# Performance work log

Measured on AMD Instinct MI355X. Metric: run time of the kernel, lower is better.

## Reference

```python
import jax, jax.numpy as jnp
import numpy as np
from functools import partial

N_NODES = 50000
N_EDGES = 800000
EMBED_DIM = 128
NUM_GROUPS = 3
T = 1.0


def setup_inputs() -> dict:
    key = jax.random.key(0)
    k1, k2, k3, k4 = jax.random.split(key, 4)
    node_feature = jax.random.normal(k1, (N_NODES, EMBED_DIM), dtype=jnp.float32)
    src = jax.random.randint(k2, (N_EDGES,), 0, N_NODES, dtype=jnp.int32)
    dst = jax.random.randint(k3, (N_EDGES,), 0, N_NODES, dtype=jnp.int32)
    W = jax.random.normal(k4, (EMBED_DIM, NUM_GROUPS), dtype=jnp.float32) / np.sqrt(EMBED_DIM)
    b = jnp.zeros((NUM_GROUPS,), dtype=jnp.float32)
    return {"node_feature": node_feature, "src": src, "dst": dst, "W": W, "b": b}


def reference(node_feature, src, dst, W, b):
    n = node_feature.shape[0]
    # linear + softmax group scores: [N, G]
    coeff = jax.nn.softmax((node_feature @ W + b) / T, axis=1)
    # weighted individual features: [N, G, D]
    wif = node_feature[:, None, :] * coeff[:, :, None]
    # message: gather src features per edge; reduce: mean over in-neighbors
    summed = jax.ops.segment_sum(wif[src], dst, num_segments=n)  # [N, G, D]
    deg = jax.ops.segment_sum(jnp.ones_like(dst, dtype=node_feature.dtype), dst, num_segments=n)
    group_feat = summed / jnp.maximum(deg, 1.0)[:, None, None]  # mean; zero-degree -> 0
    # weighted sum over groups with destination's own incidence coeff: [N, D]
    weighted_group_feat = jnp.einsum('ngd,ng->nd', group_feat, coeff)
    return weighted_group_feat
```

## Files before the change

### kernel.cpp

```cpp
#include <hip/hip_runtime.h>
#include <hip/hip_bf16.h>

#define D 128
#define G 3
#define BN 128
#define CH 8192
#define BIN_T 1024
#define CAP 4096
#define REG 8192

__global__ __launch_bounds__(256) void lg_coeff_kernel(
        const float* __restrict__ X, const float* __restrict__ W,
        const float* __restrict__ b, float4* __restrict__ coeff,
        __hip_bfloat16* __restrict__ Xh,
        int* __restrict__ cursor, int nbuck,
        int n) {
    if (cursor && blockIdx.x == 0) {
        for (int i = threadIdx.x; i < nbuck; i += 256) cursor[i] = 0;
    }
    int node = (int)((blockIdx.x * (size_t)blockDim.x + threadIdx.x) >> 6);
    int lane = threadIdx.x & 63;
    if (node >= n) return;
    float2 x = ((const float2*)(X + (size_t)node * D))[lane];
    if (Xh) {
        __hip_bfloat162 h2;
        h2.x = __float2bfloat16(x.x);
        h2.y = __float2bfloat16(x.y);
        ((__hip_bfloat162*)(Xh + (size_t)node * D))[lane] = h2;
    }
    int d0 = lane * 2;
    float s0 = x.x * W[d0 * G + 0] + x.y * W[(d0 + 1) * G + 0];
    float s1 = x.x * W[d0 * G + 1] + x.y * W[(d0 + 1) * G + 1];
    float s2 = x.x * W[d0 * G + 2] + x.y * W[(d0 + 1) * G + 2];
    #pragma unroll
    for (int off = 32; off; off >>= 1) {
        s0 += __shfl_xor(s0, off);
        s1 += __shfl_xor(s1, off);
        s2 += __shfl_xor(s2, off);
    }
    s0 += b[0]; s1 += b[1]; s2 += b[2];
    float m = fmaxf(s0, fmaxf(s1, s2));
    float e0 = __expf(s0 - m), e1 = __expf(s1 - m), e2 = __expf(s2 - m);
    float inv = 1.0f / (e0 + e1 + e2);
    if (lane == 0) coeff[node] = make_float4(e0 * inv, e1 * inv, e2 * inv, 0.0f);
}

__global__ __launch_bounds__(BIN_T) void lg_bin_kernel(
        const int* __restrict__ src, const int* __restrict__ dst,
        int* __restrict__ cursor, unsigned int* __restrict__ temp,
        int E, int nbuck) {
    __shared__ unsigned int stage[CH];
    __shared__ int hist[512], hbase[512], hcnt[512], gbs[512];
    int tid = threadIdx.x;
    int wv = tid >> 6, ln = tid & 63;
    int e0 = blockIdx.x * CH;
    int ecnt = min(CH, E - e0);
    for (int i = tid; i < 512; i += BIN_T) { hist[i] = 0; hcnt[i] = 0; }
    __syncthreads();
    int rs[CH / BIN_T], rd[CH / BIN_T];
    #pragma unroll
    for (int u = 0; u < CH / BIN_T; ++u) {
        int k = tid + u * BIN_T;
        if (k < ecnt) {
            rs[u] = src[e0 + k];
            rd[u] = dst[e0 + k];
            atomicAdd(&hist[rd[u] >> 7], 1);
        } else rd[u] = -1;
    }
    __syncthreads();
    if (wv == 0) {
        int c[8]; int tot = 0;
        #pragma unroll
        for (int t = 0; t < 8; ++t) { c[t] = hist[ln * 8 + t]; tot += c[t]; }
        int s = tot;
        #pragma unroll
        for (int o = 1; o < 64; o <<= 1) {
            int y = __shfl_up(s, o);
            if (ln >= o) s += y;
        }
        int run = s - tot;
        #pragma unroll
        for (int t = 0; t < 8; ++t) { hbase[ln * 8 + t] = run; run += c[t]; }
    }
    __syncthreads();
    #pragma unroll
    for (int u = 0; u < CH / BIN_T; ++u) {
        if (rd[u] >= 0) {
            int bk = rd[u] >> 7;
            int idx = hbase[bk] + atomicAdd(&hcnt[bk], 1);
            stage[idx] = ((unsigned int)rs[u] & 0xFFFFu) |
                         (((unsigned int)rd[u] & 127u) << 16);
        }
    }
    for (int i = tid; i < nbuck; i += BIN_T) {
        int c = hist[i];
        gbs[i] = c ? atomicAdd(&cursor[i], c) : 0;
    }
    __syncthreads();
    for (int bk = wv; bk < nbuck; bk += BIN_T / 64) {
        int c = hist[bk];
        if (!c) continue;
        int gb = gbs[bk], hb = hbase[bk];
        unsigned int* rg = temp + (size_t)bk * REG;
        int lim = min(c, REG - gb);
        for (int j = ln; j < lim; j += 64) rg[gb + j] = stage[hb + j];
    }
}

__global__ __launch_bounds__(1024) void lg_sortagg_kernel(
        const __hip_bfloat16* __restrict__ Xh,
        const float4* __restrict__ coeff,
        const unsigned int* __restrict__ temp,
        const int* __restrict__ cursor,
        float* __restrict__ out, int n) {
    __shared__ unsigned int stage[CAP];
    __shared__ float4 cdl[BN];
    __shared__ int nhist[BN], nbase[BN], ncur[BN];
    int tid = threadIdx.x;
    int wv = tid >> 6, ln = tid & 63;
    int nb0 = blockIdx.x * BN;
    int nv = min(BN, n - nb0);
    const unsigned int* rg = temp + (size_t)blockIdx.x * REG;
    int count = min(cursor[blockIdx.x], REG);
    if (tid < BN) { nhist[tid] = 0; ncur[tid] = 0; }
    if (tid < nv) cdl[tid] = coeff[nb0 + tid];
    __syncthreads();

    if (count <= CAP) {
        int k0 = tid, k1 = tid + 1024, k2 = tid + 2048, k3 = tid + 3072;
        unsigned int r0 = 0, r1 = 0, r2 = 0, r3 = 0;
        if (k0 < count) { r0 = rg[k0]; atomicAdd(&nhist[(r0 >> 16) & 127u], 1); }
        if (k1 < count) { r1 = rg[k1]; atomicAdd(&nhist[(r1 >> 16) & 127u], 1); }
        if (k2 < count) { r2 = rg[k2]; atomicAdd(&nhist[(r2 >> 16) & 127u], 1); }
        if (k3 < count) { r3 = rg[k3]; atomicAdd(&nhist[(r3 >> 16) & 127u], 1); }
        __syncthreads();
        if (wv == 0) {
            int a = nhist[2 * ln], b2 = nhist[2 * ln + 1];
            int tot = a + b2;
            int s = tot;
            #pragma unroll
            for (int o = 1; o < 64; o <<= 1) {
                int y = __shfl_up(s, o);
                if (ln >= o) s += y;
            }
            int excl = s - tot;
            nbase[2 * ln] = excl;
            nbase[2 * ln + 1] = excl + a;
        }
        __syncthreads();
        auto place = [&](unsigned int rec) {
            int s = (int)(rec & 0xFFFFu);
            int d = (int)((rec >> 16) & 127u);
            float4 cs = coeff[s];
            float4 cd = cdl[d];
            float w = cs.x * cd.x + cs.y * cd.y + cs.z * cd.z;
            unsigned int wb = __float_as_uint(w);
            wb += 0x7FFFu + ((wb >> 16) & 1u);
            int pos = nbase[d] + atomicAdd(&ncur[d], 1);
            stage[pos] = (rec & 0xFFFFu) | (wb & 0xFFFF0000u);
        };
        if (k0 < count) place(r0);
        if (k1 < count) place(r1);
        if (k2 < count) place(r2);
        if (k3 < count) place(r3);
        __syncthreads();
        for (int i = wv; i < nv; i += 16) {
            int ibeg = nbase[i];
            int icnt = nhist[i];
            float accx = 0.0f, accy = 0.0f;
            int j = 0;
            for (; j + 7 < icnt; j += 8) {
                unsigned int q0 = stage[ibeg + j + 0];
                unsigned int q1 = stage[ibeg + j + 1];
                unsigned int q2 = stage[ibeg + j + 2];
                unsigned int q3 = stage[ibeg + j + 3];
                unsigned int q4 = stage[ibeg + j + 4];
                unsigned int q5 = stage[ibeg + j + 5];
                unsigned int q6 = stage[ibeg + j + 6];
                unsigned int q7 = stage[ibeg + j + 7];
                __hip_bfloat162 h0 = ((const __hip_bfloat162*)(Xh + (size_t)(q0 & 0xFFFFu) * D))[ln];
                __hip_bfloat162 h1 = ((const __hip_bfloat162*)(Xh + (size_t)(q1 & 0xFFFFu) * D))[ln];
                __hip_bfloat162 h2 = ((const __hip_bfloat162*)(Xh + (size_t)(q2 & 0xFFFFu) * D))[ln];
                __hip_bfloat162 h3 = ((const __hip_bfloat162*)(Xh + (size_t)(q3 & 0xFFFFu) * D))[ln];
                __hip_bfloat162 h4 = ((const __hip_bfloat162*)(Xh + (size_t)(q4 & 0xFFFFu) * D))[ln];
                __hip_bfloat162 h5 = ((const __hip_bfloat162*)(Xh + (size_t)(q5 & 0xFFFFu) * D))[ln];
                __hip_bfloat162 h6 = ((const __hip_bfloat162*)(Xh + (size_t)(q6 & 0xFFFFu) * D))[ln];
                __hip_bfloat162 h7 = ((const __hip_bfloat162*)(Xh + (size_t)(q7 & 0xFFFFu) * D))[ln];
                float w0 = __uint_as_float(q0 & 0xFFFF0000u);
                float w1 = __uint_as_float(q1 & 0xFFFF0000u);
                float w2 = __uint_as_float(q2 & 0xFFFF0000u);
                float w3 = __uint_as_float(q3 & 0xFFFF0000u);
                float w4 = __uint_as_float(q4 & 0xFFFF0000u);
                float w5 = __uint_as_float(q5 & 0xFFFF0000u);
                float w6 = __uint_as_float(q6 & 0xFFFF0000u);
                float w7 = __uint_as_float(q7 & 0xFFFF0000u);
                accx = fmaf(w0, __bfloat162float(h0.x), accx);
                accy = fmaf(w0, __bfloat162float(h0.y), accy);
                accx = fmaf(w1, __bfloat162float(h1.x), accx);
                accy = fmaf(w1, __bfloat162float(h1.y), accy);
                accx = fmaf(w2, __bfloat162float(h2.x), accx);
                accy = fmaf(w2, __bfloat162float(h2.y), accy);
                accx = fmaf(w3, __bfloat162float(h3.x), accx);
                accy = fmaf(w3, __bfloat162float(h3.y), accy);
                accx = fmaf(w4, __bfloat162float(h4.x), accx);
                accy = fmaf(w4, __bfloat162float(h4.y), accy);
                accx = fmaf(w5, __bfloat162float(h5.x), accx);
                accy = fmaf(w5, __bfloat162float(h5.y), accy);
                accx = fmaf(w6, __bfloat162float(h6.x), accx);
                accy = fmaf(w6, __bfloat162float(h6.y), accy);
                accx = fmaf(w7, __bfloat162float(h7.x), accx);
                accy = fmaf(w7, __bfloat162float(h7.y), accy);
            }
            for (; j < icnt; ++j) {
                unsigned int q0 = stage[ibeg + j];
                int s0 = (int)(q0 & 0xFFFFu);
                float w0 = __uint_as_float(q0 & 0xFFFF0000u);
                __hip_bfloat162 h0 = ((const __hip_bfloat162*)(Xh + (size_t)s0 * D))[ln];
                accx = fmaf(w0, __bfloat162float(h0.x), accx);
                accy = fmaf(w0, __bfloat162float(h0.y), accy);
            }
            float invd = 1.0f / fmaxf((float)icnt, 1.0f);
            ((float2*)(out + (size_t)(nb0 + i) * D))[ln] =
                make_float2(accx * invd, accy * invd);
        }
    } else {
        for (int k = tid; k < count; k += 1024)
            atomicAdd(&nhist[(rg[k] >> 16) & 127u], 1);
        __syncthreads();
        for (int i = wv; i < nv; i += 16) {
            float4 cd = cdl[i];
            float accx = 0.0f, accy = 0.0f;
            for (int base = 0; base < count; base += 64) {
                int k = base + ln;
                unsigned int rec = (k < count) ? rg[k] : 0u;
                bool ok = (k < count) && ((int)((rec >> 16) & 127u) == i);
                unsigned long long mask = __ballot(ok);
                while (mask) {
                    int bpos = __ffsll((long long)mask) - 1;
                    mask &= mask - 1;
                    unsigned int rr = __shfl(rec, bpos);
                    int s0 = (int)(rr & 0xFFFFu);
                    float4 cs = coeff[s0];
                    float w = cs.x * cd.x + cs.y * cd.y + cs.z * cd.z;
                    __hip_bfloat162 h0 = ((const __hip_bfloat162*)(Xh + (size_t)s0 * D))[ln];
                    accx = fmaf(w, __bfloat162float(h0.x), accx);
                    accy = fmaf(w, __bfloat162float(h0.y), accy);
                }
            }
            float invd = 1.0f / fmaxf((float)nhist[i], 1.0f);
            ((float2*)(out + (size_t)(nb0 + i) * D))[ln] =
                make_float2(accx * invd, accy * invd);
        }
    }
}

__global__ void lg_deg_kernel(const int* __restrict__ dst, int* __restrict__ deg, int E) {
    int e = (int)(blockIdx.x * (size_t)blockDim.x + threadIdx.x);
    if (e < E) atomicAdd(&deg[dst[e]], 1);
}

__global__ void lg_scatter_kernel(const float* __restrict__ X,
                                  const float4* __restrict__ coeff,
                                  const int* __restrict__ src, const int* __restrict__ dst,
                                  float* __restrict__ out, int E) {
    int e = (int)((blockIdx.x * (size_t)blockDim.x + threadIdx.x) >> 6);
    int lane = threadIdx.x & 63;
    if (e >= E) return;
    int s = src[e], d = dst[e];
    float4 cs = coeff[s], cd = coeff[d];
    float se = cs.x * cd.x + cs.y * cd.y + cs.z * cd.z;
    float2 x = ((const float2*)(X + (size_t)s * D))[lane];
    atomicAdd(&out[(size_t)d * D + lane * 2 + 0], se * x.x);
    atomicAdd(&out[(size_t)d * D + lane * 2 + 1], se * x.y);
}

__global__ void lg_scale_kernel(float* __restrict__ out, const int* __restrict__ deg, int n) {
    int node = (int)((blockIdx.x * (size_t)blockDim.x + threadIdx.x) >> 6);
    int lane = threadIdx.x & 63;
    if (node >= n) return;
    float invd = 1.0f / fmaxf((float)deg[node], 1.0f);
    float2* p = (float2*)(out + (size_t)node * D);
    float2 v = p[lane];
    p[lane] = make_float2(v.x * invd, v.y * invd);
}

extern "C" void kernel_launch(void* const* d_in, const int* in_sizes, int n_in,
                              void* d_out, int out_size, void* d_ws, size_t ws_size,
                              hipStream_t stream) {
    const float* X   = (const float*)d_in[0];
    const int*   src = (const int*)d_in[1];
    const int*   dst = (const int*)d_in[2];
    const float* W   = (const float*)d_in[3];
    const float* b   = (const float*)d_in[4];
    float* out = (float*)d_out;
    int n = in_sizes[0] / D;
    int E = in_sizes[1];

    int nbuck  = (n + BN - 1) / BN;
    int nchunk = (E + CH - 1) / CH;

    char* ws = (char*)d_ws;
    size_t p = 0;
    auto alloc = [&](size_t bytes) -> void* {
        void* r = ws + p;
        p = (p + bytes + 255) & ~(size_t)255;
        return r;
    };
    float4* coeff  = (float4*)alloc((size_t)n * sizeof(float4));
    int*    cursor = (int*)alloc((size_t)nbuck * sizeof(int));
    unsigned int* temp = (unsigned int*)alloc((size_t)nbuck * REG * sizeof(unsigned int));
    __hip_bfloat16* Xh = (__hip_bfloat16*)alloc((size_t)n * D * sizeof(__hip_bfloat16));
    size_t p_full = p;
    int*    deg    = (int*)alloc((size_t)n * sizeof(int));

    int node_blocks = (n + 3) / 4;
    int edge_blocks = (E + 255) / 256;

    bool fast_ok = (n <= 65536) && (nbuck <= 512) && (p_full <= ws_size);
    if (fast_ok) {
        lg_coeff_kernel<<<node_blocks, 256, 0, stream>>>(X, W, b, coeff, Xh,
                                                         cursor, nbuck, n);
        lg_bin_kernel<<<nchunk, BIN_T, 0, stream>>>(src, dst, cursor, temp, E, nbuck);
        lg_sortagg_kernel<<<nbuck, 1024, 0, stream>>>(Xh, coeff, temp, cursor, out, n);
    } else {
        hipMemsetAsync(deg, 0, (size_t)n * sizeof(int), stream);
        hipMemsetAsync(out, 0, (size_t)n * D * sizeof(float), stream);
        lg_coeff_kernel<<<node_blocks, 256, 0, stream>>>(X, W, b, coeff, nullptr,
                                                         nullptr, 0, n);
        lg_deg_kernel<<<edge_blocks, 256, 0, stream>>>(dst, deg, E);
        lg_scatter_kernel<<<(E + 3) / 4, 256, 0, stream>>>(X, coeff, src, dst, out, E);
        lg_scale_kernel<<<node_blocks, 256, 0, stream>>>(out, deg, n);
    }
}
```

Before: 69.15 us.

## Split wave into half-waves gathering two edges with 8-byte bf16 loads

The aggregation loop now has each half-wave (32 lanes) gather a different source row with ushort4 loads, so each wave processes two edges per load instruction, then combines halves with a cross-lane shuffle before a float4 store. Bin records are loaded as uint4 per thread instead of strided scalar loads, and the binning chunk/thread constants are halved. The aim is fewer, wider memory instructions per edge, at the cost of a shuffle reduction and half the lanes idle on the store. The odd-count tail pads with a zero-weight record.

```diff
diff --git a/kernel.cpp b/kernel.cpp
--- a/kernel.cpp
+++ b/kernel.cpp
@@ -4,10 +4,14 @@
 #define D 128
 #define G 3
 #define BN 128
-#define CH 8192
-#define BIN_T 1024
+#define CH 4096
+#define BIN_T 512
 #define CAP 4096
 #define REG 8192
+
+__device__ __forceinline__ float b2f(unsigned short u) {
+    return __uint_as_float((unsigned int)u << 16);
+}
 
 __global__ __launch_bounds__(256) void lg_coeff_kernel(
         const float* __restrict__ X, const float* __restrict__ W,
@@ -127,12 +131,21 @@
     __syncthreads();
 
     if (count <= CAP) {
-        int k0 = tid, k1 = tid + 1024, k2 = tid + 2048, k3 = tid + 3072;
+        int base = tid * 4;
         unsigned int r0 = 0, r1 = 0, r2 = 0, r3 = 0;
-        if (k0 < count) { r0 = rg[k0]; atomicAdd(&nhist[(r0 >> 16) & 127u], 1); }
-        if (k1 < count) { r1 = rg[k1]; atomicAdd(&nhist[(r1 >> 16) & 127u], 1); }
-        if (k2 < count) { r2 = rg[k2]; atomicAdd(&nhist[(r2 >> 16) & 127u], 1); }
-        if (k3 < count) { r3 = rg[k3]; atomicAdd(&nhist[(r3 >> 16) & 127u], 1); }
+        if (base + 3 < count) {
+            uint4 R = *(const uint4*)(rg + base);
+            r0 = R.x; r1 = R.y; r2 = R.z; r3 = R.w;
+            atomicAdd(&nhist[(r0 >> 16) & 127u], 1);
+            atomicAdd(&nhist[(r1 >> 16) & 127u], 1);
+            atomicAdd(&nhist[(r2 >> 16) & 127u], 1);
+            atomicAdd(&nhist[(r3 >> 16) & 127u], 1);
+        } else {
+            if (base + 0 < count) { r0 = rg[base + 0]; atomicAdd(&nhist[(r0 >> 16) & 127u], 1); }
+            if (base + 1 < count) { r1 = rg[base + 1]; atomicAdd(&nhist[(r1 >> 16) & 127u], 1); }
+            if (base + 2 < count) { r2 = rg[base + 2]; atomicAdd(&nhist[(r2 >> 16) & 127u], 1); }
+            if (base + 3 < count) { r3 = rg[base + 3]; atomicAdd(&nhist[(r3 >> 16) & 127u], 1); }
+        }
         __syncthreads();
         if (wv == 0) {
             int a = nhist[2 * ln], b2 = nhist[2 * ln + 1];
@@ -159,69 +172,59 @@
             int pos = nbase[d] + atomicAdd(&ncur[d], 1);
             stage[pos] = (rec & 0xFFFFu) | (wb & 0xFFFF0000u);
         };
-        if (k0 < count) place(r0);
-        if (k1 < count) place(r1);
-        if (k2 < count) place(r2);
-        if (k3 < count) place(r3);
+        if (base + 0 < count) place(r0);
+        if (base + 1 < count) place(r1);
+        if (base + 2 < count) place(r2);
+        if (base + 3 < count) place(r3);
         __syncthreads();
+        int sub = ln & 31;
+        bool hiHalf = (ln >= 32);
         for (int i = wv; i < nv; i += 16) {
             int ibeg = nbase[i];
             int icnt = nhist[i];
-            float accx = 0.0f, accy = 0.0f;
+            float4 acc = make_float4(0.0f, 0.0f, 0.0f, 0.0f);
             int j = 0;
-            for (; j + 7 < icnt; j += 8) {
-                unsigned int q0 = stage[ibeg + j + 0];
-                unsigned int q1 = stage[ibeg + j + 1];
-                unsigned int q2 = stage[ibeg + j + 2];
-                unsigned int q3 = stage[ibeg + j + 3];
-                unsigned int q4 = stage[ibeg + j + 4];
-                unsigned int q5 = stage[ibeg + j + 5];
-                unsigned int q6 = stage[ibeg + j + 6];
-                unsigned int q7 = stage[ibeg + j + 7];
-                __hip_bfloat162 h0 = ((const __hip_bfloat162*)(Xh + (size_t)(q0 & 0xFFFFu) * D))[ln];
-                __hip_bfloat162 h1 = ((const __hip_bfloat162*)(Xh + (size_t)(q1 & 0xFFFFu) * D))[ln];
-                __hip_bfloat162 h2 = ((const __hip_bfloat162*)(Xh + (size_t)(q2 & 0xFFFFu) * D))[ln];
-                __hip_bfloat162 h3 = ((const __hip_bfloat162*)(Xh + (size_t)(q3 & 0xFFFFu) * D))[ln];
-                __hip_bfloat162 h4 = ((const __hip_bfloat162*)(Xh + (size_t)(q4 & 0xFFFFu) * D))[ln];
-                __hip_bfloat162 h5 = ((const __hip_bfloat162*)(Xh + (size_t)(q5 & 0xFFFFu) * D))[ln];
-                __hip_bfloat162 h6 = ((const __hip_bfloat162*)(Xh + (size_t)(q6 & 0xFFFFu) * D))[ln];
-                __hip_bfloat162 h7 = ((const __hip_bfloat162*)(Xh + (size_t)(q7 & 0xFFFFu) * D))[ln];
-                float w0 = __uint_as_float(q0 & 0xFFFF0000u);
-                float w1 = __uint_as_float(q1 & 0xFFFF0000u);
-                float w2 = __uint_as_float(q2 & 0xFFFF0000u);
-                float w3 = __uint_as_float(q3 & 0xFFFF0000u);
-                float w4 = __uint_as_float(q4 & 0xFFFF0000u);
-                float w5 = __uint_as_float(q5 & 0xFFFF0000u);
-                float w6 = __uint_as_float(q6 & 0xFFFF0000u);
-                float w7 = __uint_as_float(q7 & 0xFFFF0000u);
-                accx = fmaf(w0, __bfloat162float(h0.x), accx);
-                accy = fmaf(w0, __bfloat162float(h0.y), accy);
-                accx = fmaf(w1, __bfloat162float(h1.x), accx);
-                accy = fmaf(w1, __bfloat162float(h1.y), accy);
-                accx = fmaf(w2, __bfloat162float(h2.x), accx);
-                accy = fmaf(w2, __bfloat162float(h2.y), accy);
-                accx = fmaf(w3, __bfloat162float(h3.x), accx);
-                accy = fmaf(w3, __bfloat162float(h3.y), accy);
-                accx = fmaf(w4, __bfloat162float(h4.x), accx);
-                accy = fmaf(w4, __bfloat162float(h4.y), accy);
-                accx = fmaf(w5, __bfloat162float(h5.x), accx);
-                accy = fmaf(w5, __bfloat162float(h5.y), accy);
-                accx = fmaf(w6, __bfloat162float(h6.x), accx);
-                accy = fmaf(w6, __bfloat162float(h6.y), accy);
-                accx = fmaf(w7, __bfloat162float(h7.x), accx);
-                accy = fmaf(w7, __bfloat162float(h7.y), accy);
+            for (; j + 3 < icnt; j += 4) {
+                unsigned int a0 = stage[ibeg + j + 0];
+                unsigned int a1 = stage[ibeg + j + 1];
+                unsigned int b0 = stage[ibeg + j + 2];
+                unsigned int b1 = stage[ibeg + j + 3];
+                unsigned int qa = hiHalf ? a1 : a0;
+                unsigned int qb = hiHalf ? b1 : b0;
+                float wa = __uint_as_float(qa & 0xFFFF0000u);
+                float wb = __uint_as_float(qb & 0xFFFF0000u);
+                ushort4 ha = ((const ushort4*)(Xh + (size_t)(qa & 0xFFFFu) * D))[sub];
+                ushort4 hb = ((const ushort4*)(Xh + (size_t)(qb & 0xFFFFu) * D))[sub];
+                acc.x = fmaf(wa, b2f(ha.x), acc.x);
+                acc.y = fmaf(wa, b2f(ha.y), acc.y);
+                acc.z = fmaf(wa, b2f(ha.z), acc.z);
+                acc.w = fmaf(wa, b2f(ha.w), acc.w);
+                acc.x = fmaf(wb, b2f(hb.x), acc.x);
+                acc.y = fmaf(wb, b2f(hb.y), acc.y);
+                acc.z = fmaf(wb, b2f(hb.z), acc.z);
+                acc.w = fmaf(wb, b2f(hb.w), acc.w);
             }
-            for (; j < icnt; ++j) {
-                unsigned int q0 = stage[ibeg + j];
-                int s0 = (int)(q0 & 0xFFFFu);
-                float w0 = __uint_as_float(q0 & 0xFFFF0000u);
-                __hip_bfloat162 h0 = ((const __hip_bfloat162*)(Xh + (size_t)s0 * D))[ln];
-                accx = fmaf(w0, __bfloat162float(h0.x), accx);
-                accy = fmaf(w0, __bfloat162float(h0.y), accy);
+            for (; j < icnt; j += 2) {
+                unsigned int a0 = stage[ibeg + j];
+                unsigned int a1 = (j + 1 < icnt) ? stage[ibeg + j + 1]
+                                                 : (a0 & 0xFFFFu);
+                unsigned int qa = hiHalf ? a1 : a0;
+                float wa = __uint_as_float(qa & 0xFFFF0000u);
+                ushort4 ha = ((const ushort4*)(Xh + (size_t)(qa & 0xFFFFu) * D))[sub];
+                acc.x = fmaf(wa, b2f(ha.x), acc.x);
+                acc.y = fmaf(wa, b2f(ha.y), acc.y);
+                acc.z = fmaf(wa, b2f(ha.z), acc.z);
+                acc.w = fmaf(wa, b2f(ha.w), acc.w);
             }
+            acc.x += __shfl_xor(acc.x, 32);
+            acc.y += __shfl_xor(acc.y, 32);
+            acc.z += __shfl_xor(acc.z, 32);
+            acc.w += __shfl_xor(acc.w, 32);
             float invd = 1.0f / fmaxf((float)icnt, 1.0f);
-            ((float2*)(out + (size_t)(nb0 + i) * D))[ln] =
-                make_float2(accx * invd, accy * invd);
+            if (!hiHalf)
+                ((float4*)(out + (size_t)(nb0 + i) * D))[sub] =
+                    make_float4(acc.x * invd, acc.y * invd,
+                                acc.z * invd, acc.w * invd);
         }
     } else {
         for (int k = tid; k < count; k += 1024)
@@ -230,8 +233,8 @@
         for (int i = wv; i < nv; i += 16) {
             float4 cd = cdl[i];
             float accx = 0.0f, accy = 0.0f;
-            for (int base = 0; base < count; base += 64) {
-                int k = base + ln;
+            for (int bb = 0; bb < count; bb += 64) {
+                int k = bb + ln;
                 unsigned int rec = (k < count) ? rg[k] : 0u;
                 bool ok = (k < count) && ((int)((rec >> 16) & 127u) == i);
                 unsigned long long mask = __ballot(ok);
```

After: 72.88 us. 5.4% more time.
